# Optimization experiments

Hardware: AMD Instinct MI355X
Metric: run time of the kernel (lower is better)

## Reference

```python
import jax, jax.numpy as jnp
import numpy as np

B, N, C, H = 4, 8192, 1024, 16
D = C // H

def setup_inputs() -> dict:
    key = jax.random.key(0)
    k1, k2, k3 = jax.random.split(key, 3)
    scale_in = 1.0 / np.sqrt(C)
    return {
        "x": jax.random.normal(k1, (B, N, C), dtype=jnp.float32),
        "w_qkv": jax.random.normal(k2, (C, 3 * C), dtype=jnp.float32) * scale_in,
        "b_qkv": jnp.zeros((3 * C,), dtype=jnp.float32),
        "w_proj": jax.random.normal(k3, (C, C), dtype=jnp.float32) * scale_in,
        "b_proj": jnp.zeros((C,), dtype=jnp.float32),
    }

def reference(x, w_qkv, b_qkv, w_proj, b_proj):
    Bx, Nx, Cx = x.shape
    qkv = x @ w_qkv + b_qkv                       # [B,N,3C]
    qkv = qkv.reshape(Bx, Nx, 3, H, D)
    qkv = jnp.transpose(qkv, (2, 0, 3, 1, 4))     # [3,B,H,N,D]
    q, k, v = qkv[0], qkv[1], qkv[2]
    q = jax.nn.elu(q) + 1.0                       # positive feature map
    k = jax.nn.elu(k) + 1.0
    kv = jnp.einsum('bhnd,bhne->bhde', k, v)      # [B,H,D,D]
    out = jnp.einsum('bhnd,bhde->bhne', q, kv)    # [B,H,N,D]
    z = 1.0 / (jnp.einsum('bhnd,bhd->bhn', q, k.sum(axis=2)) + 1e-8)
    out = out * z[..., None]
    out = jnp.transpose(out, (0, 2, 1, 3)).reshape(Bx, Nx, Cx)
    out = out @ w_proj + b_proj                   # dropout is identity in eval
    return out
```

## Files before the change

### kernel.cpp

```cpp
#include <hip/hip_runtime.h>
#include <hip/hip_bf16.h>
#include <stdint.h>

typedef unsigned short ushort_t;
typedef __attribute__((ext_vector_type(8))) short short8;
typedef __attribute__((ext_vector_type(4))) float floatx4;

__device__ __forceinline__ ushort_t f2b(float f) {
    unsigned u = __float_as_uint(f);
    unsigned r = (u + 0x7FFFu + ((u >> 16) & 1u)) >> 16;
    return (ushort_t)r;
}
__device__ __forceinline__ float b2f(ushort_t h) {
    return __uint_as_float(((unsigned)h) << 16);
}

#define GLDS16(srcp, dstp)                                                          \
    __builtin_amdgcn_global_load_lds(                                               \
        (const __attribute__((address_space(1))) unsigned int*)(srcp),              \
        (__attribute__((address_space(3))) unsigned int*)(dstp), 16, 0, 0)


__global__ void conv_bf16(const float* __restrict__ in, ushort_t* __restrict__ out, int n8) {
    for (int i = blockIdx.x * blockDim.x + threadIdx.x; i < n8; i += gridDim.x * blockDim.x) {
        const float4 f0 = *(const float4*)&in[(size_t)i * 8];
        const float4 f1 = *(const float4*)&in[(size_t)i * 8 + 4];
        ushort4 o0, o1;
        o0.x = f2b(f0.x); o0.y = f2b(f0.y); o0.z = f2b(f0.z); o0.w = f2b(f0.w);
        o1.x = f2b(f1.x); o1.y = f2b(f1.y); o1.z = f2b(f1.z); o1.w = f2b(f1.w);
        *(ushort4*)&out[(size_t)i * 8]     = o0;
        *(ushort4*)&out[(size_t)i * 8 + 4] = o1;
    }
}

__global__ void transpose_conv(const float* __restrict__ in, ushort_t* __restrict__ out,
                               int R, int C) {
    __shared__ float tile[32][33];
    int c0 = blockIdx.x * 32, r0 = blockIdx.y * 32;
    int tx = threadIdx.x, ty = threadIdx.y;
#pragma unroll
    for (int k = 0; k < 4; ++k) {
        int a = ty * 4 + k;
        tile[a][tx] = in[(size_t)(r0 + a) * C + c0 + tx];
    }
    __syncthreads();
#pragma unroll
    for (int k = 0; k < 4; ++k) {
        int a = ty * 4 + k;
        out[(size_t)(c0 + a) * R + r0 + tx] = f2b(tile[tx][a]);
    }
}

__global__ void zero_f32(float* __restrict__ p, int n) {
    int i = blockIdx.x * blockDim.x + threadIdx.x;
    if (i < n) p[i] = 0.f;
}

template<int MODE>
__global__ __launch_bounds__(512, 2) void gemm256(
    const ushort_t* __restrict__ A, const ushort_t* __restrict__ Bt,
    const float* __restrict__ bias,
    ushort_t* __restrict__ out_u16, float* __restrict__ out_f32,
    int Nt, int nbx)
{
    extern __shared__ ushort_t lds[];
    constexpr int KK = 1024;

    const int tid  = threadIdx.x;
    const int wave = tid >> 6;
    const int lane = tid & 63;
    const int wm_i = wave >> 2;
    const int wn_i = wave & 3;
    const int fr   = lane & 15;
    const int fq   = lane >> 4;

    const int nwg = (int)gridDim.x;
    const int bid = (int)blockIdx.x;
    const int swz = (bid & 7) * (nwg >> 3) + (bid >> 3);
    const int bx = swz % nbx, by = swz / nbx;
    const int m0 = by * 256, n0 = bx * 256;

    const int trow = tid >> 3;
    const int csw  = ((tid & 7) ^ (trow & 7)) << 3;
    const int tcolB = ((tid >> 8) << 6) + (trow & 31);

    const ushort_t* sa = A  + (size_t)(m0 + trow)  * KK + csw;
    const ushort_t* sb = Bt + (size_t)(n0 + tcolB) * KK + csw;

    const int dstA = wave * 512;
    const int dstB = 16384 + wave * 512;

    const int sw0 = (fq ^ (fr & 7)) << 3;
    const int sw1 = sw0 ^ 32;
    const int abase = (wm_i * 64 + fr) * 64;
    const int bbase = (wn_i * 32 + fr) * 64;
    int loA0[2][2], loA1[2][2], loB0[2][2], loB1[2][2];
#pragma unroll
    for (int bf = 0; bf < 2; ++bf)
#pragma unroll
        for (int q = 0; q < 2; ++q) {
            loA0[bf][q] = bf * 32768 + q * 8192 + abase + sw0;
            loA1[bf][q] = bf * 32768 + q * 8192 + abase + sw1;
            loB0[bf][q] = bf * 32768 + 16384 + q * 8192 + bbase + sw0;
            loB1[bf][q] = bf * 32768 + 16384 + q * 8192 + bbase + sw1;
        }

    floatx4 acc[8][4];
    const floatx4 z4 = {0.f, 0.f, 0.f, 0.f};
#pragma unroll
    for (int i = 0; i < 8; ++i)
#pragma unroll
        for (int j = 0; j < 4; ++j) acc[i][j] = z4;

    short8 a[4][2], b[2][2];

    auto stageA = [&](int buf, int h, int ko) {
        ushort_t* d = lds + buf * 32768 + h * 8192 + dstA;
        GLDS16(sa + h * (64 * KK) + ko, d);
        GLDS16(sa + h * (64 * KK) + 128 * KK + ko, d + 4096);
    };
    auto stageB = [&](int buf, int h, int ko) {
        ushort_t* d = lds + buf * 32768 + h * 8192 + dstB;
        GLDS16(sb + h * (32 * KK) + ko, d);
        GLDS16(sb + h * (32 * KK) + 128 * KK + ko, d + 4096);
    };
    auto loadA = [&](int buf, int qr) {
        const int o0 = loA0[buf][qr], o1 = loA1[buf][qr];
#pragma unroll
        for (int i = 0; i < 4; ++i) {
            a[i][0] = *(const short8*)(lds + o0 + i * 1024);
            a[i][1] = *(const short8*)(lds + o1 + i * 1024);
        }
    };
    auto loadB = [&](int buf, int qc) {
        const int o0 = loB0[buf][qc], o1 = loB1[buf][qc];
#pragma unroll
        for (int j = 0; j < 2; ++j) {
            b[j][0] = *(const short8*)(lds + o0 + j * 1024);
            b[j][1] = *(const short8*)(lds + o1 + j * 1024);
        }
    };
    auto mma = [&](int qr, int qc) {
#pragma unroll
        for (int i = 0; i < 4; ++i)
#pragma unroll
            for (int j = 0; j < 2; ++j) {
                acc[qr * 4 + i][qc * 2 + j] =
                    __builtin_amdgcn_mfma_f32_16x16x32_bf16(a[i][0], b[j][0], acc[qr * 4 + i][qc * 2 + j], 0, 0, 0);
                acc[qr * 4 + i][qc * 2 + j] =
                    __builtin_amdgcn_mfma_f32_16x16x32_bf16(a[i][1], b[j][1], acc[qr * 4 + i][qc * 2 + j], 0, 0, 0);
            }
    };

#define BIN()  __builtin_amdgcn_s_barrier(); __builtin_amdgcn_s_setprio(1)
#define BOUT() __builtin_amdgcn_s_setprio(0); __builtin_amdgcn_s_barrier()
#define VM6()  asm volatile("s_waitcnt vmcnt(6)" ::: "memory")
#define VM0()  asm volatile("s_waitcnt vmcnt(0)" ::: "memory")

    stageA(0, 0, 0);
    stageB(0, 1, 0);
    stageA(0, 1, 0);
    stageB(0, 0, 0);
    stageA(1, 0, 64);
    stageB(1, 1, 64);
    stageA(1, 1, 64);
    VM6();
    __builtin_amdgcn_s_barrier();

    int ko = 0;
    for (int pr = 0; pr < 7; ++pr, ko += 128) {
        loadA(0, 0); loadB(0, 0);
        stageB(1, 0, ko + 64);
        BIN(); mma(0, 0); BOUT();

        loadB(0, 1);
        stageA(0, 0, ko + 128);
        BIN(); mma(0, 1); BOUT();

        loadA(0, 1);
        stageB(0, 1, ko + 128);
        BIN(); mma(1, 1); BOUT();

        loadB(0, 0);
        stageA(0, 1, ko + 128);
        BIN(); mma(1, 0); VM6(); BOUT();

        loadA(1, 0); loadB(1, 0);
        stageB(0, 0, ko + 128);
        BIN(); mma(0, 0); BOUT();

        loadB(1, 1);
        stageA(1, 0, ko + 192);
        BIN(); mma(0, 1); BOUT();

        loadA(1, 1);
        stageB(1, 1, ko + 192);
        BIN(); mma(1, 1); BOUT();

        loadB(1, 0);
        stageA(1, 1, ko + 192);
        BIN(); mma(1, 0); VM6(); BOUT();
    }

    loadA(0, 0); loadB(0, 0);
    stageB(1, 0, 960);
    BIN(); mma(0, 0); BOUT();

    loadB(0, 1);
    BIN(); mma(0, 1); BOUT();

    loadA(0, 1);
    BIN(); mma(1, 1); BOUT();

    loadB(0, 0);
    BIN(); mma(1, 0); VM0(); BOUT();

    loadA(1, 0); loadB(1, 0);
    BIN(); mma(0, 0); BOUT();

    loadB(1, 1);
    BIN(); mma(0, 1); BOUT();

    loadA(1, 1);
    BIN(); mma(1, 1); BOUT();

    loadB(1, 0);
    BIN(); mma(1, 0);
    __builtin_amdgcn_s_setprio(0);

#undef BIN
#undef BOUT
#undef VM6
#undef VM0

#pragma unroll
    for (int ri = 0; ri < 8; ++ri) {
#pragma unroll
        for (int cj = 0; cj < 4; ++cj) {
            const int col = n0 + wn_i * 64 + (cj >> 1) * 32 + (cj & 1) * 16 + fr;
            const float bv = bias[col];
            const int rowb = m0 + wm_i * 128 + (ri >> 2) * 64 + (ri & 3) * 16 + fq * 4;
            if (MODE == 0) {
                const int s = col >> 10;
                const int c = col & 1023;
                const int h = c >> 6;
                const int d = c & 63;
#pragma unroll
                for (int r = 0; r < 4; ++r) {
                    const int row = rowb + r;
                    const int bb = row >> 13;
                    const int n  = row & 8191;
                    float v = acc[ri][cj][r] + bv;
                    if (s < 2) v = (v > 0.f) ? (v + 1.f) : __expf(v);
                    out_u16[(((size_t)s * 64 + bb * 16 + h) * 8192 + n) * 64 + d] = f2b(v);
                }
            } else {
#pragma unroll
                for (int r = 0; r < 4; ++r) {
                    const int row = rowb + r;
                    out_f32[(size_t)row * Nt + col] = acc[ri][cj][r] + bv;
                }
            }
        }
    }
}

__global__ __launch_bounds__(256) void kv_kernel(
    const ushort_t* __restrict__ kbuf, const ushort_t* __restrict__ vbuf,
    float* __restrict__ kv, float* __restrict__ ksum)
{
    __shared__ ushort_t ks[64 * 64] __attribute__((aligned(16)));
    __shared__ ushort_t vs[64 * 64] __attribute__((aligned(16)));

    const int bh = blockIdx.y, chunk = blockIdx.x, t = threadIdx.x;
    const int d0 = (t >> 4) * 4, e0 = (t & 15) * 4;
    const bool do_ksum = (t & 15) == 0;

    float acc[4][4];
#pragma unroll
    for (int i = 0; i < 4; ++i)
#pragma unroll
        for (int j = 0; j < 4; ++j) acc[i][j] = 0.f;
    float kacc[4] = {0.f, 0.f, 0.f, 0.f};

    for (int sub = 0; sub < 8; ++sub) {
        const int nb = chunk * 512 + sub * 64;
        __syncthreads();
#pragma unroll
        for (int p = 0; p < 2; ++p) {
            int idx = p * 256 + t;
            int r = idx >> 3, c = (idx & 7) * 8;
            *(short8*)&ks[r * 64 + c] = *(const short8*)&kbuf[((size_t)bh * 8192 + nb + r) * 64 + c];
            *(short8*)&vs[r * 64 + c] = *(const short8*)&vbuf[((size_t)bh * 8192 + nb + r) * 64 + c];
        }
        __syncthreads();
        for (int n = 0; n < 64; ++n) {
            ushort4 kd = *(const ushort4*)&ks[n * 64 + d0];
            ushort4 ve = *(const ushort4*)&vs[n * 64 + e0];
            float kf[4] = {b2f(kd.x), b2f(kd.y), b2f(kd.z), b2f(kd.w)};
            float vf[4] = {b2f(ve.x), b2f(ve.y), b2f(ve.z), b2f(ve.w)};
#pragma unroll
            for (int i = 0; i < 4; ++i) {
#pragma unroll
                for (int j = 0; j < 4; ++j) acc[i][j] += kf[i] * vf[j];
            }
            if (do_ksum) {
#pragma unroll
                for (int i = 0; i < 4; ++i) kacc[i] += kf[i];
            }
        }
    }
#pragma unroll
    for (int i = 0; i < 4; ++i) {
        if (do_ksum) atomicAdd(&ksum[bh * 64 + d0 + i], kacc[i]);
#pragma unroll
        for (int j = 0; j < 4; ++j)
            atomicAdd(&kv[((size_t)bh * 64 + d0 + i) * 64 + e0 + j], acc[i][j]);
    }
}

__global__ __launch_bounds__(256) void out_kernel(
    const ushort_t* __restrict__ qbuf, const float* __restrict__ kv,
    const float* __restrict__ ksum, ushort_t* __restrict__ obuf)
{
    __shared__ float kvs[4096];
    __shared__ float ksums[64];
    __shared__ float qs[16][65];

    const int bh = blockIdx.y, chunk = blockIdx.x, t = threadIdx.x;
    const int b = bh >> 4, h = bh & 15;
    const int myrow = t >> 4, e0 = (t & 15) * 4;

#pragma unroll
    for (int i = 0; i < 4; ++i) {
        int idx = (i * 256 + t) * 4;
        *(float4*)&kvs[idx] = *(const float4*)&kv[(size_t)bh * 4096 + idx];
    }
    if (t < 64) ksums[t] = ksum[bh * 64 + t];

    for (int pass = 0; pass < 8; ++pass) {
        const int n = chunk * 128 + pass * 16 + myrow;
        __syncthreads();
        {
            int col = (t & 15) * 4;
            ushort4 qv4 = *(const ushort4*)&qbuf[((size_t)bh * 8192 + chunk * 128 + pass * 16 + myrow) * 64 + col];
            qs[myrow][col + 0] = b2f(qv4.x);
            qs[myrow][col + 1] = b2f(qv4.y);
            qs[myrow][col + 2] = b2f(qv4.z);
            qs[myrow][col + 3] = b2f(qv4.w);
        }
        __syncthreads();
        float a0 = 0.f, a1 = 0.f, a2 = 0.f, a3 = 0.f, z = 0.f;
        for (int d = 0; d < 64; ++d) {
            const float qv = qs[myrow][d];
            const float4 kvv = *(const float4*)&kvs[d * 64 + e0];
            a0 += qv * kvv.x; a1 += qv * kvv.y; a2 += qv * kvv.z; a3 += qv * kvv.w;
            z += qv * ksums[d];
        }
        const float zi = 1.f / (z + 1e-8f);
        ushort4 o;
        o.x = f2b(a0 * zi); o.y = f2b(a1 * zi); o.z = f2b(a2 * zi); o.w = f2b(a3 * zi);
        *(ushort4*)&obuf[((size_t)b * 8192 + n) * 1024 + h * 64 + e0] = o;
    }
}


extern "C" void kernel_launch(void* const* d_in, const int* in_sizes, int n_in,
                              void* d_out, int out_size, void* d_ws, size_t ws_size,
                              hipStream_t stream) {
    const float* x      = (const float*)d_in[0];
    const float* w_qkv  = (const float*)d_in[1];
    const float* b_qkv  = (const float*)d_in[2];
    const float* w_proj = (const float*)d_in[3];
    const float* b_proj = (const float*)d_in[4];
    float* out = (float*)d_out;

    const size_t XE = (size_t)32768 * 1024;

    char* ws = (char*)d_ws;
    ushort_t* xb   = (ushort_t*)ws;  ws += XE * 2;
    ushort_t* wqT  = (ushort_t*)ws;  ws += (size_t)3072 * 1024 * 2;
    ushort_t* wpT  = (ushort_t*)ws;  ws += (size_t)1024 * 1024 * 2;
    ushort_t* qkvb = (ushort_t*)ws;  ws += 3 * XE * 2;
    ushort_t* ob   = (ushort_t*)ws;  ws += XE * 2;
    float*    kv   = (float*)ws;     ws += (size_t)64 * 64 * 64 * 4;
    float*    ksum = (float*)ws;     ws += (size_t)64 * 64 * 4;

    (void)hipFuncSetAttribute(reinterpret_cast<const void*>(gemm256<0>),
                              hipFuncAttributeMaxDynamicSharedMemorySize, 131072);
    (void)hipFuncSetAttribute(reinterpret_cast<const void*>(gemm256<1>),
                              hipFuncAttributeMaxDynamicSharedMemorySize, 131072);

    zero_f32<<<dim3((64 * 64 * 64 + 64 * 64 + 255) / 256), dim3(256), 0, stream>>>(kv, 64 * 64 * 64 + 64 * 64);
    conv_bf16<<<dim3(2048), dim3(256), 0, stream>>>(x, xb, (int)(XE / 8));
    transpose_conv<<<dim3(96, 32), dim3(32, 8), 0, stream>>>(w_qkv, wqT, 1024, 3072);
    transpose_conv<<<dim3(32, 32), dim3(32, 8), 0, stream>>>(w_proj, wpT, 1024, 1024);

    gemm256<0><<<dim3(1536), dim3(512), 131072, stream>>>(xb, wqT, b_qkv, qkvb, nullptr, 3072, 12);

    kv_kernel<<<dim3(16, 64), dim3(256), 0, stream>>>(qkvb + XE, qkvb + 2 * XE, kv, ksum);
    out_kernel<<<dim3(64, 64), dim3(256), 0, stream>>>(qkvb, kv, ksum, ob);

    gemm256<1><<<dim3(512), dim3(512), 131072, stream>>>(ob, wpT, b_proj, nullptr, out, 1024, 4);
}
```

Baseline: 545.2 us.

## Store QKV row-major with vectorized epilogue and move ELU into attention kernels

```diff
diff --git a/kernel.cpp b/kernel.cpp
--- a/kernel.cpp
+++ b/kernel.cpp
@@ -13,6 +13,9 @@
 }
 __device__ __forceinline__ float b2f(ushort_t h) {
     return __uint_as_float(((unsigned)h) << 16);
+}
+__device__ __forceinline__ float elu1(float f) {
+    return (f > 0.f) ? (f + 1.f) : __expf(f);
 }
 
 #define GLDS16(srcp, dstp)                                                          \
@@ -146,16 +149,16 @@
 #pragma unroll
             for (int j = 0; j < 2; ++j) {
                 acc[qr * 4 + i][qc * 2 + j] =
-                    __builtin_amdgcn_mfma_f32_16x16x32_bf16(a[i][0], b[j][0], acc[qr * 4 + i][qc * 2 + j], 0, 0, 0);
+                    __builtin_amdgcn_mfma_f32_16x16x32_bf16(b[j][0], a[i][0], acc[qr * 4 + i][qc * 2 + j], 0, 0, 0);
                 acc[qr * 4 + i][qc * 2 + j] =
-                    __builtin_amdgcn_mfma_f32_16x16x32_bf16(a[i][1], b[j][1], acc[qr * 4 + i][qc * 2 + j], 0, 0, 0);
+                    __builtin_amdgcn_mfma_f32_16x16x32_bf16(b[j][1], a[i][1], acc[qr * 4 + i][qc * 2 + j], 0, 0, 0);
             }
     };
 
-#define BIN()  __builtin_amdgcn_s_barrier(); __builtin_amdgcn_s_setprio(1)
-#define BOUT() __builtin_amdgcn_s_setprio(0); __builtin_amdgcn_s_barrier()
-#define VM6()  asm volatile("s_waitcnt vmcnt(6)" ::: "memory")
-#define VM0()  asm volatile("s_waitcnt vmcnt(0)" ::: "memory")
+#define PRIO1() __builtin_amdgcn_s_setprio(1)
+#define BOUT()  __builtin_amdgcn_s_setprio(0); __builtin_amdgcn_s_barrier()
+#define VM6()   asm volatile("s_waitcnt vmcnt(6)" ::: "memory")
+#define VM0()   asm volatile("s_waitcnt vmcnt(0)" ::: "memory")
 
     stageA(0, 0, 0);
     stageB(0, 1, 0);
@@ -171,110 +174,116 @@
     for (int pr = 0; pr < 7; ++pr, ko += 128) {
         loadA(0, 0); loadB(0, 0);
         stageB(1, 0, ko + 64);
-        BIN(); mma(0, 0); BOUT();
+        PRIO1(); mma(0, 0); BOUT();
 
         loadB(0, 1);
         stageA(0, 0, ko + 128);
-        BIN(); mma(0, 1); BOUT();
+        PRIO1(); mma(0, 1); BOUT();
 
         loadA(0, 1);
         stageB(0, 1, ko + 128);
-        BIN(); mma(1, 1); BOUT();
+        PRIO1(); mma(1, 1); BOUT();
 
         loadB(0, 0);
         stageA(0, 1, ko + 128);
-        BIN(); mma(1, 0); VM6(); BOUT();
+        PRIO1(); mma(1, 0); __builtin_amdgcn_s_setprio(0); VM6();
+        __builtin_amdgcn_s_barrier();
 
         loadA(1, 0); loadB(1, 0);
         stageB(0, 0, ko + 128);
-        BIN(); mma(0, 0); BOUT();
+        PRIO1(); mma(0, 0); BOUT();
 
         loadB(1, 1);
         stageA(1, 0, ko + 192);
-        BIN(); mma(0, 1); BOUT();
+        PRIO1(); mma(0, 1); BOUT();
 
         loadA(1, 1);
         stageB(1, 1, ko + 192);
-        BIN(); mma(1, 1); BOUT();
+        PRIO1(); mma(1, 1); BOUT();
 
         loadB(1, 0);
         stageA(1, 1, ko + 192);
-        BIN(); mma(1, 0); VM6(); BOUT();
+        PRIO1(); mma(1, 0); __builtin_amdgcn_s_setprio(0); VM6();
+        __builtin_amdgcn_s_barrier();
     }
 
     loadA(0, 0); loadB(0, 0);
     stageB(1, 0, 960);
-    BIN(); mma(0, 0); BOUT();
+    PRIO1(); mma(0, 0); BOUT();
 
     loadB(0, 1);
-    BIN(); mma(0, 1); BOUT();
+    PRIO1(); mma(0, 1); BOUT();
 
     loadA(0, 1);
-    BIN(); mma(1, 1); BOUT();
+    PRIO1(); mma(1, 1); BOUT();
 
     loadB(0, 0);
-    BIN(); mma(1, 0); VM0(); BOUT();
+    PRIO1(); mma(1, 0); __builtin_amdgcn_s_setprio(0); VM0();
+    __builtin_amdgcn_s_barrier();
 
     loadA(1, 0); loadB(1, 0);
-    BIN(); mma(0, 0); BOUT();
+    PRIO1(); mma(0, 0); BOUT();
 
     loadB(1, 1);
-    BIN(); mma(0, 1); BOUT();
+    PRIO1(); mma(0, 1); BOUT();
 
     loadA(1, 1);
-    BIN(); mma(1, 1); BOUT();
+    PRIO1(); mma(1, 1); BOUT();
 
     loadB(1, 0);
-    BIN(); mma(1, 0);
+    PRIO1(); mma(1, 0);
     __builtin_amdgcn_s_setprio(0);
 
-#undef BIN
+#undef PRIO1
 #undef BOUT
 #undef VM6
 #undef VM0
 
+    float4 bv[4];
+#pragma unroll
+    for (int cj = 0; cj < 4; ++cj) {
+        const int nb = n0 + wn_i * 64 + (cj >> 1) * 32 + (cj & 1) * 16 + fq * 4;
+        bv[cj] = *(const float4*)&bias[nb];
+    }
 #pragma unroll
     for (int ri = 0; ri < 8; ++ri) {
+        const int m = m0 + wm_i * 128 + (ri >> 2) * 64 + (ri & 3) * 16 + fr;
 #pragma unroll
         for (int cj = 0; cj < 4; ++cj) {
-            const int col = n0 + wn_i * 64 + (cj >> 1) * 32 + (cj & 1) * 16 + fr;
-            const float bv = bias[col];
-            const int rowb = m0 + wm_i * 128 + (ri >> 2) * 64 + (ri & 3) * 16 + fq * 4;
+            const int nb = n0 + wn_i * 64 + (cj >> 1) * 32 + (cj & 1) * 16 + fq * 4;
             if (MODE == 0) {
-                const int s = col >> 10;
-                const int c = col & 1023;
-                const int h = c >> 6;
-                const int d = c & 63;
-#pragma unroll
-                for (int r = 0; r < 4; ++r) {
-                    const int row = rowb + r;
-                    const int bb = row >> 13;
-                    const int n  = row & 8191;
-                    float v = acc[ri][cj][r] + bv;
-                    if (s < 2) v = (v > 0.f) ? (v + 1.f) : __expf(v);
-                    out_u16[(((size_t)s * 64 + bb * 16 + h) * 8192 + n) * 64 + d] = f2b(v);
-                }
+                ushort4 o;
+                o.x = f2b(acc[ri][cj][0] + bv[cj].x);
+                o.y = f2b(acc[ri][cj][1] + bv[cj].y);
+                o.z = f2b(acc[ri][cj][2] + bv[cj].z);
+                o.w = f2b(acc[ri][cj][3] + bv[cj].w);
+                *(ushort4*)&out_u16[(size_t)m * Nt + nb] = o;
             } else {
-#pragma unroll
-                for (int r = 0; r < 4; ++r) {
-                    const int row = rowb + r;
-                    out_f32[(size_t)row * Nt + col] = acc[ri][cj][r] + bv;
-                }
+                float4 o;
+                o.x = acc[ri][cj][0] + bv[cj].x;
+                o.y = acc[ri][cj][1] + bv[cj].y;
+                o.z = acc[ri][cj][2] + bv[cj].z;
+                o.w = acc[ri][cj][3] + bv[cj].w;
+                *(float4*)&out_f32[(size_t)m * Nt + nb] = o;
             }
         }
     }
 }
 
 __global__ __launch_bounds__(256) void kv_kernel(
-    const ushort_t* __restrict__ kbuf, const ushort_t* __restrict__ vbuf,
+    const ushort_t* __restrict__ qkvb,
     float* __restrict__ kv, float* __restrict__ ksum)
 {
     __shared__ ushort_t ks[64 * 64] __attribute__((aligned(16)));
     __shared__ ushort_t vs[64 * 64] __attribute__((aligned(16)));
 
     const int bh = blockIdx.y, chunk = blockIdx.x, t = threadIdx.x;
+    const int b = bh >> 4, h = bh & 15;
     const int d0 = (t >> 4) * 4, e0 = (t & 15) * 4;
     const bool do_ksum = (t & 15) == 0;
+
+    const int sr = t >> 2;
+    const int sc = (t & 3) * 16;
 
     float acc[4][4];
 #pragma unroll
@@ -286,12 +295,20 @@
     for (int sub = 0; sub < 8; ++sub) {
         const int nb = chunk * 512 + sub * 64;
         __syncthreads();
-#pragma unroll
-        for (int p = 0; p < 2; ++p) {
-            int idx = p * 256 + t;
-            int r = idx >> 3, c = (idx & 7) * 8;
-            *(short8*)&ks[r * 64 + c] = *(const short8*)&kbuf[((size_t)bh * 8192 + nb + r) * 64 + c];
-            *(short8*)&vs[r * 64 + c] = *(const short8*)&vbuf[((size_t)bh * 8192 + nb + r) * 64 + c];
+        {
+            const ushort_t* row = qkvb + ((size_t)b * 8192 + nb + sr) * 3072 + h * 64 + sc;
+            short8 k0 = *(const short8*)(row + 1024);
+            short8 k1 = *(const short8*)(row + 1024 + 8);
+            short8 ko0, ko1;
+#pragma unroll
+            for (int i = 0; i < 8; ++i) {
+                ko0[i] = (short)f2b(elu1(b2f((ushort_t)k0[i])));
+                ko1[i] = (short)f2b(elu1(b2f((ushort_t)k1[i])));
+            }
+            *(short8*)&ks[sr * 64 + sc]     = ko0;
+            *(short8*)&ks[sr * 64 + sc + 8] = ko1;
+            *(short8*)&vs[sr * 64 + sc]     = *(const short8*)(row + 2048);
+            *(short8*)&vs[sr * 64 + sc + 8] = *(const short8*)(row + 2048 + 8);
         }
         __syncthreads();
         for (int n = 0; n < 64; ++n) {
@@ -320,7 +337,7 @@
 }
 
 __global__ __launch_bounds__(256) void out_kernel(
-    const ushort_t* __restrict__ qbuf, const float* __restrict__ kv,
+    const ushort_t* __restrict__ qkvb, const float* __restrict__ kv,
     const float* __restrict__ ksum, ushort_t* __restrict__ obuf)
 {
     __shared__ float kvs[4096];
@@ -343,11 +360,11 @@
         __syncthreads();
         {
             int col = (t & 15) * 4;
-            ushort4 qv4 = *(const ushort4*)&qbuf[((size_t)bh * 8192 + chunk * 128 + pass * 16 + myrow) * 64 + col];
-            qs[myrow][col + 0] = b2f(qv4.x);
-            qs[myrow][col + 1] = b2f(qv4.y);
-            qs[myrow][col + 2] = b2f(qv4.z);
-            qs[myrow][col + 3] = b2f(qv4.w);
+            ushort4 qv4 = *(const ushort4*)&qkvb[((size_t)b * 8192 + n) * 3072 + h * 64 + col];
+            qs[myrow][col + 0] = elu1(b2f(qv4.x));
+            qs[myrow][col + 1] = elu1(b2f(qv4.y));
+            qs[myrow][col + 2] = elu1(b2f(qv4.z));
+            qs[myrow][col + 3] = elu1(b2f(qv4.w));
         }
         __syncthreads();
         float a0 = 0.f, a1 = 0.f, a2 = 0.f, a3 = 0.f, z = 0.f;
@@ -398,7 +415,7 @@
 
     gemm256<0><<<dim3(1536), dim3(512), 131072, stream>>>(xb, wqT, b_qkv, qkvb, nullptr, 3072, 12);
 
-    kv_kernel<<<dim3(16, 64), dim3(256), 0, stream>>>(qkvb + XE, qkvb + 2 * XE, kv, ksum);
+    kv_kernel<<<dim3(16, 64), dim3(256), 0, stream>>>(qkvb, kv, ksum);
     out_kernel<<<dim3(64, 64), dim3(256), 0, stream>>>(qkvb, kv, ksum, ob);
 
     gemm256<1><<<dim3(512), dim3(512), 131072, stream>>>(ob, wpT, b_proj, nullptr, out, 1024, 4);
```

After: 559.9 us. 1.03x slower.
